# Optimization experiments

Measured on AMD Instinct MI355X. Metric: run time of the kernel, lower is better.

Reference implementation:

```python
import jax, jax.numpy as jnp
import numpy as np

P = 4        # patch_size
H = 16       # num_heads
C = 32       # num_channels
E = C * P ** 3  # embed dim = 2048


def setup_inputs() -> dict:
    key = jax.random.key(0)
    ks = jax.random.split(key, 6)
    s = 0.02
    x = jax.random.normal(ks[0], (4, C, 64, 64, 64), dtype=jnp.float32)
    in_proj_w = jax.random.normal(ks[1], (3 * E, E), dtype=jnp.float32) * s
    in_proj_b = jnp.zeros((3 * E,), dtype=jnp.float32)
    out_proj_w = jax.random.normal(ks[2], (E, E), dtype=jnp.float32) * s
    out_proj_b = jnp.zeros((E,), dtype=jnp.float32)
    mlp_w = jax.random.normal(ks[3], (E, E), dtype=jnp.float32) * s
    mlp_b = jnp.zeros((E,), dtype=jnp.float32)
    return {"x": x, "in_proj_w": in_proj_w, "in_proj_b": in_proj_b,
            "out_proj_w": out_proj_w, "out_proj_b": out_proj_b,
            "mlp_w": mlp_w, "mlp_b": mlp_b}


def reference(x, in_proj_w, in_proj_b, out_proj_w, out_proj_b, mlp_w, mlp_b):
    B, Cc, Rx, Ry, Rz = x.shape
    Nx, Ny, Nz = Rx // P, Ry // P, Rz // P
    N = Nx * Ny * Nz
    hd = E // H

    # --- window partition (torch unfold x3) -> (B, C, Nx, Ny, Nz, px, py, pz)
    xw = x.reshape(B, Cc, Nx, P, Ny, P, Nz, P).transpose(0, 1, 2, 4, 6, 3, 5, 7)
    # -> (B, N, C*p^3); torch then feeds MHA with batch_first=False,
    # so seq_len = B and batch = N (attention mixes across the B axis!)
    tok = xw.reshape(B, Cc, N, P, P, P).transpose(0, 2, 1, 3, 4, 5).reshape(B, N, E)

    # --- multi-head attention (seq = B, batch = N)
    qkv = tok @ in_proj_w.T + in_proj_b            # (B, N, 3E)
    q, k, v = jnp.split(qkv, 3, axis=-1)
    q = q.reshape(B, N, H, hd)
    k = k.reshape(B, N, H, hd)
    v = v.reshape(B, N, H, hd)
    scale = 1.0 / jnp.sqrt(jnp.asarray(hd, dtype=q.dtype))
    scores = jnp.einsum('snhd,tnhd->nhst', q * scale, k)   # (N, H, B, B)
    attn = jax.nn.softmax(scores, axis=-1)
    o = jnp.einsum('nhst,tnhd->snhd', attn, v).reshape(B, N, E)
    o = o @ out_proj_w.T + out_proj_b

    # --- mlp
    o = o @ mlp_w.T + mlp_b

    # --- window reverse, matching the torch.cat-based reassembly:
    # out[b,c, px*Nx+nx, py*Ny+ny, pz*Nz+nz] = x8[b,c,nx,ny,nz,px,py,pz]
    x8 = o.reshape(B, N, Cc, P, P, P).transpose(0, 2, 1, 3, 4, 5)
    x8 = x8.reshape(B, Cc, Nx, Ny, Nz, P, P, P)
    out = x8.transpose(0, 1, 5, 2, 6, 3, 7, 4).reshape(B, Cc, Rx, Ry, Rz)
    return out
```

## Files before the change

### kernel.cpp

```cpp
#include <hip/hip_runtime.h>
#include <stdio.h>


typedef __attribute__((ext_vector_type(4))) float f32x4;
typedef __attribute__((ext_vector_type(8))) short s16x8;
typedef __attribute__((ext_vector_type(2))) unsigned short u16x2;
typedef __attribute__((ext_vector_type(4))) unsigned short u16x4;

#define NB 4
#define NC 32
#define NTOK 4096
#define ED 2048
#define NH 16
#define HD 128

__device__ __forceinline__ unsigned short f2bf(float f) {
    union { float f; unsigned int u; } v; v.f = f;
    unsigned int r = (v.u + 0x7fffu + ((v.u >> 16) & 1u)) >> 16;
    return (unsigned short)r;
}
__device__ __forceinline__ float bf2f(unsigned short u) {
    union { unsigned int u; float f; } v; v.u = ((unsigned int)u) << 16;
    return v.f;
}

#define BARRIER() asm volatile("s_barrier" ::: "memory")
#define LGKM0() do { asm volatile("s_waitcnt lgkmcnt(0)" ::: "memory"); \
                     __builtin_amdgcn_sched_barrier(0); } while (0)
#define VMCNT(n) asm volatile("s_waitcnt vmcnt(" #n ")" ::: "memory")

__global__ void f32_to_bf16_kernel(const float* __restrict__ src,
                                   unsigned short* __restrict__ dst, int n4) {
    int i = blockIdx.x * blockDim.x + threadIdx.x;
    if (i >= n4) return;
    f32x4 v = *(const f32x4*)(src + (size_t)i * 4);
    u16x4 w;
    w.x = f2bf(v.x); w.y = f2bf(v.y); w.z = f2bf(v.z); w.w = f2bf(v.w);
    *(u16x4*)(dst + (size_t)i * 4) = w;
}

__global__ __launch_bounds__(256) void transpose_bf16_kernel(
    const float* __restrict__ src, unsigned short* __restrict__ dst, int n) {
    __shared__ float lds[64][68];
    const int bx = blockIdx.x * 64;
    const int by = blockIdx.y * 64;
    const int t  = threadIdx.x;
    const int r  = t >> 2;
    const int c4 = (t & 3) * 16;
    const float* s = src + (size_t)(by + r) * n + bx + c4;
    #pragma unroll
    for (int i = 0; i < 4; ++i)
        *(f32x4*)&lds[r][c4 + i * 4] = *(const f32x4*)(s + i * 4);
    __syncthreads();
    unsigned short* d = dst + (size_t)(bx + r) * n + by + c4;
    #pragma unroll
    for (int i = 0; i < 4; ++i) {
        u16x4 w;
        w.x = f2bf(lds[c4 + i * 4 + 0][r]);
        w.y = f2bf(lds[c4 + i * 4 + 1][r]);
        w.z = f2bf(lds[c4 + i * 4 + 2][r]);
        w.w = f2bf(lds[c4 + i * 4 + 3][r]);
        *(u16x4*)(d + i * 4) = w;
    }
}

__global__ void bcomb_kernel(const float* __restrict__ mlp_w,
                             const float* __restrict__ opb,
                             const float* __restrict__ mlpb,
                             float* __restrict__ bcomb) {
    int i = blockIdx.x * blockDim.x + threadIdx.x;
    const float* row = mlp_w + (size_t)i * ED;
    float s = 0.0f;
    for (int k = 0; k < ED; k += 4) {
        f32x4 a = *(const f32x4*)(row + k);
        f32x4 b = *(const f32x4*)(opb + k);
        s += a.x * b.x + a.y * b.y + a.z * b.z + a.w * b.w;
    }
    bcomb[i] = s + mlpb[i];
}

__global__ void partition_kernel(const float* __restrict__ x,
                                 unsigned short* __restrict__ tok) {
    int idx = blockIdx.x * blockDim.x + threadIdx.x;
    int m = idx & 15;
    int t = idx >> 4;
    int Y = t & 63; t >>= 6;
    int X = t & 63; t >>= 6;
    int c = t & 31;
    int b = t >> 5;
    f32x4 xv = *(const f32x4*)(x + (size_t)idx * 4);
    int nx = X >> 2, px = X & 3;
    int ny = Y >> 2, py = Y & 3;
    int n = nx * 256 + ny * 16 + m;
    int e = c * 64 + px * 16 + py * 4;
    size_t dst = (size_t)(b * NTOK + n) * ED + e;
    u16x4 w;
    w.x = f2bf(xv.x); w.y = f2bf(xv.y); w.z = f2bf(xv.z); w.w = f2bf(xv.w);
    *(u16x4*)&tok[dst] = w;
}

__global__ __launch_bounds__(256) void gemm128(
    const unsigned short* __restrict__ A,
    const unsigned short* __restrict__ W,
    const float* __restrict__ bias,
    unsigned short* __restrict__ C,
    int M, int Nout, int K)
{
    __shared__ unsigned short ldsA[128 * 64];
    __shared__ unsigned short ldsW[128 * 64];

    const int tid  = threadIdx.x;
    const int wave = tid >> 6;
    const int lane = tid & 63;
    const int bm = blockIdx.x * 128;
    const int bn = blockIdx.y * 128;
    const int wm = (wave >> 1) * 64;
    const int wn = (wave & 1) * 64;

    f32x4 acc[4][4] = {};

    const int srow = lane >> 3;
    const int scol = (lane & 7) * 8;
    const int lrow = lane & 15;
    const int lk   = (lane >> 4) * 8;

    const int nkt = K >> 6;
    for (int kt = 0; kt < nkt; ++kt) {
        const int kbase = kt * 64;
        #pragma unroll
        for (int q = 0; q < 4; ++q) {
            int chunk = wave * 4 + q;
            int row = chunk * 8 + srow;
            const unsigned short* ga = A + (size_t)(bm + row) * K + kbase + scol;
            const unsigned short* gw = W + (size_t)(bn + row) * K + kbase + scol;
            __builtin_amdgcn_global_load_lds(
                (const __attribute__((address_space(1))) void*)ga,
                (__attribute__((address_space(3))) void*)(&ldsA[chunk * 512]),
                16, 0, 0);
            __builtin_amdgcn_global_load_lds(
                (const __attribute__((address_space(1))) void*)gw,
                (__attribute__((address_space(3))) void*)(&ldsW[chunk * 512]),
                16, 0, 0);
        }
        __syncthreads();

        #pragma unroll
        for (int ks = 0; ks < 2; ++ks) {
            const int k0 = ks * 32 + lk;
            s16x8 af[4], bf[4];
            #pragma unroll
            for (int m = 0; m < 4; ++m)
                af[m] = *(const s16x8*)&ldsA[(wm + m * 16 + lrow) * 64 + k0];
            #pragma unroll
            for (int n = 0; n < 4; ++n)
                bf[n] = *(const s16x8*)&ldsW[(wn + n * 16 + lrow) * 64 + k0];
            #pragma unroll
            for (int m = 0; m < 4; ++m)
                #pragma unroll
                for (int n = 0; n < 4; ++n)
                    acc[m][n] = __builtin_amdgcn_mfma_f32_16x16x32_bf16(
                        af[m], bf[n], acc[m][n], 0, 0, 0);
        }
        __syncthreads();
    }

    const int col   = lane & 15;
    const int rbase = (lane >> 4) * 4;
    #pragma unroll
    for (int n = 0; n < 4; ++n) {
        int cc = bn + wn + n * 16 + col;
        float bv = bias[cc];
        #pragma unroll
        for (int m = 0; m < 4; ++m)
            #pragma unroll
            for (int r = 0; r < 4; ++r) {
                int rr = bm + wm + m * 16 + rbase + r;
                C[(size_t)rr * Nout + cc] = f2bf(acc[m][n][r] + bv);
            }
    }
}

template <int OUT_BF16>
__global__ __launch_bounds__(512, 2) void gemm256(
    const unsigned short* __restrict__ A,
    const unsigned short* __restrict__ W,
    const float* __restrict__ bias,
    void* __restrict__ Cv,
    int M, int Nout, int K)
{
    __shared__ unsigned short ldsA[2][2][128 * 64];
    __shared__ unsigned short ldsB[2][2][128 * 64];

    const int tid  = threadIdx.x;
    const int wave = tid >> 6;
    const int lane = tid & 63;

    const int f   = blockIdx.x;
    const int xcd = f & 7;
    const int r_  = f >> 3;
    const int mac = r_ >> 5;
    const int w_  = r_ & 31;
    const int bm  = (xcd * 8 + (w_ & 7)) * 256;
    const int bn  = (mac * 4 + (w_ >> 3)) * 256;

    const int wi    = wave >> 2;
    const int wj    = wave & 3;
    const int bhalf = wj >> 1;
    const int bcol  = (wj & 1) * 64;

    const int lrow = lane & 15;
    const int kq   = lane >> 4;
    const int s0   = ((kq ^ (lrow & 7)) << 3);

    f32x4 acc[8][4] = {};

    const int nkt = K >> 6;

    const int srl   = lane >> 3;
    const int sslot = (((lane & 7) ^ srl) << 3);

    auto stA = [&](int db, int half, int tt) {
        const unsigned short* gb = A + (size_t)(bm + half * 128) * K + tt * 64;
        unsigned short* lb = &ldsA[db][half][0];
        #pragma unroll
        for (int q = 0; q < 2; ++q) {
            const int r0 = wave * 16 + q * 8;
            const unsigned short* ga = gb + (size_t)(r0 + srl) * K + sslot;
            __builtin_amdgcn_global_load_lds(
                (const __attribute__((address_space(1))) void*)ga,
                (__attribute__((address_space(3))) void*)(lb + r0 * 64),
                16, 0, 0);
        }
    };
    auto stB = [&](int db, int half, int tt) {
        const unsigned short* gb = W + (size_t)(bn + half * 128) * K + tt * 64;
        unsigned short* lb = &ldsB[db][half][0];
        #pragma unroll
        for (int q = 0; q < 2; ++q) {
            const int r0 = wave * 16 + q * 8;
            const unsigned short* ga = gb + (size_t)(r0 + srl) * K + sslot;
            __builtin_amdgcn_global_load_lds(
                (const __attribute__((address_space(1))) void*)ga,
                (__attribute__((address_space(3))) void*)(lb + r0 * 64),
                16, 0, 0);
        }
    };

    stA(0, 0, 0); stA(0, 1, 0);
    stB(0, 0, 0); stB(0, 1, 0);
    stA(1, 0, 1); stA(1, 1, 1);
    VMCNT(4);
    BARRIER();

    for (int t = 0; t < nkt; ++t) {
        const int db = t & 1;
        const unsigned short* hA = &ldsA[db][wi][0];
        const unsigned short* hB = &ldsB[db][bhalf][0];

        s16x8 a[8][2], bl[2][2], bh[2][2];

        #pragma unroll
        for (int m = 0; m < 8; ++m) {
            const int rb = (m * 16 + lrow) * 64;
            a[m][0] = *(const s16x8*)&hA[rb + s0];
            a[m][1] = *(const s16x8*)&hA[rb + (s0 ^ 32)];
        }
        #pragma unroll
        for (int n = 0; n < 2; ++n) {
            const int rb = (bcol + n * 16 + lrow) * 64;
            bl[n][0] = *(const s16x8*)&hB[rb + s0];
            bl[n][1] = *(const s16x8*)&hB[rb + (s0 ^ 32)];
        }
        if (t + 1 < nkt) { stB(db ^ 1, 0, t + 1); stB(db ^ 1, 1, t + 1); }
        LGKM0();
        __builtin_amdgcn_s_setprio(1);
        #pragma unroll
        for (int m = 0; m < 8; ++m)
            #pragma unroll
            for (int n = 0; n < 2; ++n) {
                acc[m][n] = __builtin_amdgcn_mfma_f32_16x16x32_bf16(a[m][0], bl[n][0], acc[m][n], 0, 0, 0);
                acc[m][n] = __builtin_amdgcn_mfma_f32_16x16x32_bf16(a[m][1], bl[n][1], acc[m][n], 0, 0, 0);
            }
        __builtin_amdgcn_s_setprio(0);
        BARRIER();

        #pragma unroll
        for (int n = 0; n < 2; ++n) {
            const int rb = (bcol + (n + 2) * 16 + lrow) * 64;
            bh[n][0] = *(const s16x8*)&hB[rb + s0];
            bh[n][1] = *(const s16x8*)&hB[rb + (s0 ^ 32)];
        }
        if (t + 2 < nkt) { stA(db, 0, t + 2); stA(db, 1, t + 2); }
        LGKM0();
        __builtin_amdgcn_s_setprio(1);
        #pragma unroll
        for (int m = 0; m < 8; ++m)
            #pragma unroll
            for (int n = 0; n < 2; ++n) {
                acc[m][n + 2] = __builtin_amdgcn_mfma_f32_16x16x32_bf16(a[m][0], bh[n][0], acc[m][n + 2], 0, 0, 0);
                acc[m][n + 2] = __builtin_amdgcn_mfma_f32_16x16x32_bf16(a[m][1], bh[n][1], acc[m][n + 2], 0, 0, 0);
            }
        __builtin_amdgcn_s_setprio(0);
        if (t + 2 < nkt)      { VMCNT(4); }
        else                  { VMCNT(0); }
        BARRIER();
    }

    const int rowbase = bm + wi * 128 + (kq << 2);
    const int colbase = bn + wj * 64 + lrow;
    float bv[4];
    #pragma unroll
    for (int n = 0; n < 4; ++n) bv[n] = bias[colbase + n * 16];
    #pragma unroll
    for (int m = 0; m < 8; ++m) {
        #pragma unroll
        for (int r = 0; r < 4; ++r) {
            const int rr = rowbase + m * 16 + r;
            #pragma unroll
            for (int n = 0; n < 4; ++n) {
                const int cc = colbase + n * 16;
                const float val = acc[m][n][r] + bv[n];
                if (OUT_BF16)
                    ((unsigned short*)Cv)[(size_t)rr * Nout + cc] = f2bf(val);
                else
                    ((float*)Cv)[(size_t)rr * Nout + cc] = val;
            }
        }
    }
}

__global__ __launch_bounds__(64) void attn_kernel(
    const unsigned short* __restrict__ qkv, unsigned short* __restrict__ o)
{
    const int bid  = blockIdx.x;
    const int n    = bid >> 4;
    const int h    = bid & 15;
    const int lane = threadIdx.x;
    const int d0   = lane * 2;
    const float scale = 0.0883883476483184405501f;

    float q[4][2], k[4][2], v[4][2];
    #pragma unroll
    for (int b = 0; b < 4; ++b) {
        size_t base = (size_t)(b * NTOK + n) * (3 * ED) + h * HD + d0;
        u16x2 uq = *(const u16x2*)&qkv[base];
        u16x2 uk = *(const u16x2*)&qkv[base + ED];
        u16x2 uv = *(const u16x2*)&qkv[base + 2 * ED];
        q[b][0] = bf2f(uq.x); q[b][1] = bf2f(uq.y);
        k[b][0] = bf2f(uk.x); k[b][1] = bf2f(uk.y);
        v[b][0] = bf2f(uv.x); v[b][1] = bf2f(uv.y);
    }

    float sc[4][4];
    #pragma unroll
    for (int s = 0; s < 4; ++s) {
        #pragma unroll
        for (int t = 0; t < 4; ++t) {
            float p = q[s][0] * k[t][0] + q[s][1] * k[t][1];
            #pragma unroll
            for (int off = 32; off > 0; off >>= 1)
                p += __shfl_xor(p, off, 64);
            sc[s][t] = p * scale;
        }
    }

    #pragma unroll
    for (int s = 0; s < 4; ++s) {
        float mx = fmaxf(fmaxf(sc[s][0], sc[s][1]), fmaxf(sc[s][2], sc[s][3]));
        float e0 = __expf(sc[s][0] - mx);
        float e1 = __expf(sc[s][1] - mx);
        float e2 = __expf(sc[s][2] - mx);
        float e3 = __expf(sc[s][3] - mx);
        float inv = 1.0f / (e0 + e1 + e2 + e3);
        float o0 = (e0 * v[0][0] + e1 * v[1][0] + e2 * v[2][0] + e3 * v[3][0]) * inv;
        float o1 = (e0 * v[0][1] + e1 * v[1][1] + e2 * v[2][1] + e3 * v[3][1]) * inv;
        size_t ob = (size_t)(s * NTOK + n) * ED + h * HD + d0;
        u16x2 ov; ov.x = f2bf(o0); ov.y = f2bf(o1);
        *(u16x2*)&o[ob] = ov;
    }
}

__global__ __launch_bounds__(256) void reverse_kernel(const float* __restrict__ o3,
                                                      float* __restrict__ out) {
    __shared__ float lds[16][2052];
    const int t  = threadIdx.x;
    const int b  = blockIdx.x >> 8;
    const int nx = (blockIdx.x >> 4) & 15;
    const int ny = blockIdx.x & 15;
    const int n0 = nx * 256 + ny * 16;

    {
        const int row = t >> 4;
        const int cb  = (t & 15) * 128;
        const float* src = o3 + (size_t)(b * NTOK + n0 + row) * ED + cb;
        #pragma unroll
        for (int i = 0; i < 32; ++i)
            *(f32x4*)&lds[row][cb + i * 4] = *(const f32x4*)&src[i * 4];
    }
    __syncthreads();

    #pragma unroll
    for (int j = 0; j < 2; ++j) {
        const int id = t + j * 256;
        const int py = id & 3, px = (id >> 2) & 3, c = id >> 4;
        const int eb = c * 64 + px * 16 + py * 4;
        f32x4 v[16];
        #pragma unroll
        for (int nz = 0; nz < 16; ++nz)
            v[nz] = *(const f32x4*)&lds[nz][eb];
        float* ob = out + ((size_t)(b * NC + c) * 64 + px * 16 + nx) * 4096
                        + (size_t)(py * 16 + ny) * 64;
        #pragma unroll
        for (int pz = 0; pz < 4; ++pz) {
            float* oz = ob + pz * 16;
            f32x4 w0 = {v[0][pz],  v[1][pz],  v[2][pz],  v[3][pz]};
            f32x4 w1 = {v[4][pz],  v[5][pz],  v[6][pz],  v[7][pz]};
            f32x4 w2 = {v[8][pz],  v[9][pz],  v[10][pz], v[11][pz]};
            f32x4 w3 = {v[12][pz], v[13][pz], v[14][pz], v[15][pz]};
            *(f32x4*)&oz[0]  = w0; *(f32x4*)&oz[4]  = w1;
            *(f32x4*)&oz[8]  = w2; *(f32x4*)&oz[12] = w3;
        }
    }
}

extern "C" void kernel_launch(void* const* d_in, const int* in_sizes, int n_in,
                              void* d_out, int out_size, void* d_ws, size_t ws_size,
                              hipStream_t stream) {
    const float* x          = (const float*)d_in[0];
    const float* in_proj_w  = (const float*)d_in[1];
    const float* in_proj_b  = (const float*)d_in[2];
    const float* out_proj_w = (const float*)d_in[3];
    const float* out_proj_b = (const float*)d_in[4];
    const float* mlp_w      = (const float*)d_in[5];
    const float* mlp_b      = (const float*)d_in[6];
    float* out = (float*)d_out;

    const size_t M = 16384;
    char* ws = (char*)d_ws;
    size_t off = 0;
    unsigned short* tok    = (unsigned short*)(ws + off); off += M * ED * 2;
    unsigned short* w_in   = (unsigned short*)(ws + off); off += (size_t)3 * ED * ED * 2;
    unsigned short* w_mlp  = (unsigned short*)(ws + off); off += (size_t)ED * ED * 2;
    unsigned short* w_outT = (unsigned short*)(ws + off); off += (size_t)ED * ED * 2;
    unsigned short* w_comb = (unsigned short*)(ws + off); off += (size_t)ED * ED * 2;
    float* zbias           = (float*)(ws + off);          off += ED * 4;
    float* b_comb          = (float*)(ws + off);          off += ED * 4;
    unsigned short* obuf   = (unsigned short*)(ws + off); off += M * ED * 2;
    unsigned short* qkv    = (unsigned short*)(ws + off); off += M * 3 * ED * 2;
    float* o3 = (float*)qkv;

    if (ws_size < off) {
        fprintf(stderr, "kernel_launch: ws too small (%zu < %zu)\n", ws_size, off);
        return;
    }

    {
        int n4 = 3 * ED * ED / 4;
        f32_to_bf16_kernel<<<(n4 + 255) / 256, 256, 0, stream>>>(in_proj_w, w_in, n4);
        n4 = ED * ED / 4;
        f32_to_bf16_kernel<<<(n4 + 255) / 256, 256, 0, stream>>>(mlp_w, w_mlp, n4);
        transpose_bf16_kernel<<<dim3(ED / 64, ED / 64), 256, 0, stream>>>(
            out_proj_w, w_outT, ED);
        hipMemsetAsync(zbias, 0, ED * sizeof(float), stream);
    }

    gemm128<<<dim3(ED / 128, ED / 128), 256, 0, stream>>>(
        w_mlp, w_outT, zbias, w_comb, ED, ED, ED);
    bcomb_kernel<<<ED / 256, 256, 0, stream>>>(mlp_w, out_proj_b, mlp_b, b_comb);

    partition_kernel<<<(NB * NC * 64 * 64 * 16) / 256, 256, 0, stream>>>(x, tok);

    gemm256<1><<<dim3(64 * (6144 / 256)), 512, 0, stream>>>(
        tok, w_in, in_proj_b, qkv, 16384, 6144, 2048);

    attn_kernel<<<NTOK * NH, 64, 0, stream>>>(qkv, obuf);

    gemm256<0><<<dim3(64 * (2048 / 256)), 512, 0, stream>>>(
        obuf, w_comb, b_comb, o3, 16384, 2048, 2048);

    reverse_kernel<<<NB * 16 * 16, 256, 0, stream>>>(o3, out);
}
```

Before: 803.0 us.

## Restructure GEMM main loop to prefetch next tile's A fragments during MFMA

Reorganizes the bf16 GEMM inner loop so that A and B tiles for step t+2 are issued together into one double buffer. The low half of the A fragments for the next k-step is loaded from LDS before the second MFMA block, overlapping LDS reads with matrix math. The MFMA work is split by A row halves rather than B column halves, and a partial lgkmcnt wait lets the first MFMAs start while the aHi reads are still in flight. This adds register pressure from the carried aLo fragments, an extra barrier per iteration, and relies on the buffer-reuse ordering staying correct.

```diff
diff --git a/kernel.cpp b/kernel.cpp
--- a/kernel.cpp
+++ b/kernel.cpp
@@ -26,6 +26,8 @@
 
 #define BARRIER() asm volatile("s_barrier" ::: "memory")
 #define LGKM0() do { asm volatile("s_waitcnt lgkmcnt(0)" ::: "memory"); \
+                     __builtin_amdgcn_sched_barrier(0); } while (0)
+#define LGKM8() do { asm volatile("s_waitcnt lgkmcnt(8)" ::: "memory"); \
                      __builtin_amdgcn_sched_barrier(0); } while (0)
 #define VMCNT(n) asm volatile("s_waitcnt vmcnt(" #n ")" ::: "memory")
 
@@ -246,64 +248,98 @@
         }
     };
 
-    stA(0, 0, 0); stA(0, 1, 0);
-    stB(0, 0, 0); stB(0, 1, 0);
-    stA(1, 0, 1); stA(1, 1, 1);
-    VMCNT(4);
+    stA(0, 0, 0); stA(0, 1, 0); stB(0, 0, 0); stB(0, 1, 0);
+    stA(1, 0, 1); stA(1, 1, 1); stB(1, 0, 1); stB(1, 1, 1);
+    VMCNT(8);
     BARRIER();
+
+    s16x8 aLo[4][2];
+    {
+        const unsigned short* hA0 = &ldsA[0][wi][0];
+        #pragma unroll
+        for (int m = 0; m < 4; ++m) {
+            const int rb = (m * 16 + lrow) * 64;
+            aLo[m][0] = *(const s16x8*)&hA0[rb + s0];
+            aLo[m][1] = *(const s16x8*)&hA0[rb + (s0 ^ 32)];
+        }
+    }
 
     for (int t = 0; t < nkt; ++t) {
         const int db = t & 1;
         const unsigned short* hA = &ldsA[db][wi][0];
         const unsigned short* hB = &ldsB[db][bhalf][0];
 
-        s16x8 a[8][2], bl[2][2], bh[2][2];
-
-        #pragma unroll
-        for (int m = 0; m < 8; ++m) {
-            const int rb = (m * 16 + lrow) * 64;
-            a[m][0] = *(const s16x8*)&hA[rb + s0];
-            a[m][1] = *(const s16x8*)&hA[rb + (s0 ^ 32)];
-        }
+        s16x8 aHi[4][2], bl[2][2], bh[2][2];
+
+        LGKM0();
         #pragma unroll
         for (int n = 0; n < 2; ++n) {
             const int rb = (bcol + n * 16 + lrow) * 64;
             bl[n][0] = *(const s16x8*)&hB[rb + s0];
             bl[n][1] = *(const s16x8*)&hB[rb + (s0 ^ 32)];
         }
-        if (t + 1 < nkt) { stB(db ^ 1, 0, t + 1); stB(db ^ 1, 1, t + 1); }
-        LGKM0();
-        __builtin_amdgcn_s_setprio(1);
-        #pragma unroll
-        for (int m = 0; m < 8; ++m)
-            #pragma unroll
-            for (int n = 0; n < 2; ++n) {
-                acc[m][n] = __builtin_amdgcn_mfma_f32_16x16x32_bf16(a[m][0], bl[n][0], acc[m][n], 0, 0, 0);
-                acc[m][n] = __builtin_amdgcn_mfma_f32_16x16x32_bf16(a[m][1], bl[n][1], acc[m][n], 0, 0, 0);
-            }
-        __builtin_amdgcn_s_setprio(0);
-        BARRIER();
-
         #pragma unroll
         for (int n = 0; n < 2; ++n) {
             const int rb = (bcol + (n + 2) * 16 + lrow) * 64;
             bh[n][0] = *(const s16x8*)&hB[rb + s0];
             bh[n][1] = *(const s16x8*)&hB[rb + (s0 ^ 32)];
         }
-        if (t + 2 < nkt) { stA(db, 0, t + 2); stA(db, 1, t + 2); }
-        LGKM0();
+        __builtin_amdgcn_sched_barrier(0);
+        #pragma unroll
+        for (int m = 0; m < 4; ++m) {
+            const int rb = ((m + 4) * 16 + lrow) * 64;
+            aHi[m][0] = *(const s16x8*)&hA[rb + s0];
+            aHi[m][1] = *(const s16x8*)&hA[rb + (s0 ^ 32)];
+        }
+        LGKM8();
+
         __builtin_amdgcn_s_setprio(1);
         #pragma unroll
-        for (int m = 0; m < 8; ++m)
+        for (int m = 0; m < 4; ++m)
             #pragma unroll
             for (int n = 0; n < 2; ++n) {
-                acc[m][n + 2] = __builtin_amdgcn_mfma_f32_16x16x32_bf16(a[m][0], bh[n][0], acc[m][n + 2], 0, 0, 0);
-                acc[m][n + 2] = __builtin_amdgcn_mfma_f32_16x16x32_bf16(a[m][1], bh[n][1], acc[m][n + 2], 0, 0, 0);
+                acc[m][n]     = __builtin_amdgcn_mfma_f32_16x16x32_bf16(aLo[m][0], bl[n][0], acc[m][n], 0, 0, 0);
+                acc[m][n]     = __builtin_amdgcn_mfma_f32_16x16x32_bf16(aLo[m][1], bl[n][1], acc[m][n], 0, 0, 0);
+                acc[m][n + 2] = __builtin_amdgcn_mfma_f32_16x16x32_bf16(aLo[m][0], bh[n][0], acc[m][n + 2], 0, 0, 0);
+                acc[m][n + 2] = __builtin_amdgcn_mfma_f32_16x16x32_bf16(aLo[m][1], bh[n][1], acc[m][n + 2], 0, 0, 0);
             }
         __builtin_amdgcn_s_setprio(0);
-        if (t + 2 < nkt)      { VMCNT(4); }
-        else                  { VMCNT(0); }
+        __builtin_amdgcn_sched_barrier(0);
+
+        LGKM0();
         BARRIER();
+
+        if (t + 2 < nkt) {
+            stA(db, 0, t + 2); stA(db, 1, t + 2);
+            stB(db, 0, t + 2); stB(db, 1, t + 2);
+            VMCNT(8);
+        } else {
+            VMCNT(0);
+        }
+        BARRIER();
+
+        if (t + 1 < nkt) {
+            const unsigned short* hA2 = &ldsA[db ^ 1][wi][0];
+            #pragma unroll
+            for (int m = 0; m < 4; ++m) {
+                const int rb = (m * 16 + lrow) * 64;
+                aLo[m][0] = *(const s16x8*)&hA2[rb + s0];
+                aLo[m][1] = *(const s16x8*)&hA2[rb + (s0 ^ 32)];
+            }
+        }
+        __builtin_amdgcn_sched_barrier(0);
+
+        __builtin_amdgcn_s_setprio(1);
+        #pragma unroll
+        for (int m = 0; m < 4; ++m)
+            #pragma unroll
+            for (int n = 0; n < 2; ++n) {
+                acc[m + 4][n]     = __builtin_amdgcn_mfma_f32_16x16x32_bf16(aHi[m][0], bl[n][0], acc[m + 4][n], 0, 0, 0);
+                acc[m + 4][n]     = __builtin_amdgcn_mfma_f32_16x16x32_bf16(aHi[m][1], bl[n][1], acc[m + 4][n], 0, 0, 0);
+                acc[m + 4][n + 2] = __builtin_amdgcn_mfma_f32_16x16x32_bf16(aHi[m][0], bh[n][0], acc[m + 4][n + 2], 0, 0, 0);
+                acc[m + 4][n + 2] = __builtin_amdgcn_mfma_f32_16x16x32_bf16(aHi[m][1], bh[n][1], acc[m + 4][n + 2], 0, 0, 0);
+            }
+        __builtin_amdgcn_s_setprio(0);
     }
 
     const int rowbase = bm + wi * 128 + (kq << 2);
```

Result: slower. 984.5 us (+22.6%).

## Split gemm256 inner loop into quadrants to overlap LDS reads with MFMA

Applied to the files above, without the earlier changes.

The main K-loop of gemm256 now loads the A fragments in two halves and issues MFMAs in four quadrants. This interleaves LDS reads with matrix math, replacing one lgkmcnt wait and one barrier with scheduling seams, and lowers peak register pressure. Separately, the bias-combination kernel now uses one wave per row with a shuffle reduction instead of one thread per row, giving far more parallelism and coalesced loads. The risk is that the looser waits misorder LDS reads against the asynchronous stores into the other buffer, and that compiler scheduling across the seams turns out worse.

```diff
diff --git a/kernel.cpp b/kernel.cpp
--- a/kernel.cpp
+++ b/kernel.cpp
@@ -28,6 +28,7 @@
 #define LGKM0() do { asm volatile("s_waitcnt lgkmcnt(0)" ::: "memory"); \
                      __builtin_amdgcn_sched_barrier(0); } while (0)
 #define VMCNT(n) asm volatile("s_waitcnt vmcnt(" #n ")" ::: "memory")
+#define SEAM() __builtin_amdgcn_sched_barrier(0)
 
 __global__ void f32_to_bf16_kernel(const float* __restrict__ src,
                                    unsigned short* __restrict__ dst, int n4) {
@@ -64,19 +65,21 @@
     }
 }
 
-__global__ void bcomb_kernel(const float* __restrict__ mlp_w,
-                             const float* __restrict__ opb,
-                             const float* __restrict__ mlpb,
-                             float* __restrict__ bcomb) {
-    int i = blockIdx.x * blockDim.x + threadIdx.x;
-    const float* row = mlp_w + (size_t)i * ED;
+__global__ __launch_bounds__(256) void bcomb_kernel(
+    const float* __restrict__ mlp_w, const float* __restrict__ opb,
+    const float* __restrict__ mlpb, float* __restrict__ bcomb) {
+    const int wave = threadIdx.x >> 6, lane = threadIdx.x & 63;
+    const int row = blockIdx.x * 4 + wave;
+    const float* r = mlp_w + (size_t)row * ED;
     float s = 0.0f;
-    for (int k = 0; k < ED; k += 4) {
-        f32x4 a = *(const f32x4*)(row + k);
+    for (int k = lane * 4; k < ED; k += 256) {
+        f32x4 a = *(const f32x4*)(r + k);
         f32x4 b = *(const f32x4*)(opb + k);
         s += a.x * b.x + a.y * b.y + a.z * b.z + a.w * b.w;
     }
-    bcomb[i] = s + mlpb[i];
+    #pragma unroll
+    for (int off = 32; off > 0; off >>= 1) s += __shfl_xor(s, off, 64);
+    if (lane == 0) bcomb[row] = s + mlpb[row];
 }
 
 __global__ void partition_kernel(const float* __restrict__ x,
@@ -257,13 +260,13 @@
         const unsigned short* hA = &ldsA[db][wi][0];
         const unsigned short* hB = &ldsB[db][bhalf][0];
 
-        s16x8 a[8][2], bl[2][2], bh[2][2];
-
-        #pragma unroll
-        for (int m = 0; m < 8; ++m) {
+        s16x8 aLo[4][2], aHi[4][2], bl[2][2], bh[2][2];
+
+        #pragma unroll
+        for (int m = 0; m < 4; ++m) {
             const int rb = (m * 16 + lrow) * 64;
-            a[m][0] = *(const s16x8*)&hA[rb + s0];
-            a[m][1] = *(const s16x8*)&hA[rb + (s0 ^ 32)];
+            aLo[m][0] = *(const s16x8*)&hA[rb + s0];
+            aLo[m][1] = *(const s16x8*)&hA[rb + (s0 ^ 32)];
         }
         #pragma unroll
         for (int n = 0; n < 2; ++n) {
@@ -272,17 +275,17 @@
             bl[n][1] = *(const s16x8*)&hB[rb + (s0 ^ 32)];
         }
         if (t + 1 < nkt) { stB(db ^ 1, 0, t + 1); stB(db ^ 1, 1, t + 1); }
-        LGKM0();
+        SEAM();
         __builtin_amdgcn_s_setprio(1);
         #pragma unroll
-        for (int m = 0; m < 8; ++m)
+        for (int m = 0; m < 4; ++m)
             #pragma unroll
             for (int n = 0; n < 2; ++n) {
-                acc[m][n] = __builtin_amdgcn_mfma_f32_16x16x32_bf16(a[m][0], bl[n][0], acc[m][n], 0, 0, 0);
-                acc[m][n] = __builtin_amdgcn_mfma_f32_16x16x32_bf16(a[m][1], bl[n][1], acc[m][n], 0, 0, 0);
+                acc[m][n] = __builtin_amdgcn_mfma_f32_16x16x32_bf16(aLo[m][0], bl[n][0], acc[m][n], 0, 0, 0);
+                acc[m][n] = __builtin_amdgcn_mfma_f32_16x16x32_bf16(aLo[m][1], bl[n][1], acc[m][n], 0, 0, 0);
             }
         __builtin_amdgcn_s_setprio(0);
-        BARRIER();
+        SEAM();
 
         #pragma unroll
         for (int n = 0; n < 2; ++n) {
@@ -290,15 +293,44 @@
             bh[n][0] = *(const s16x8*)&hB[rb + s0];
             bh[n][1] = *(const s16x8*)&hB[rb + (s0 ^ 32)];
         }
+        __builtin_amdgcn_s_setprio(1);
+        #pragma unroll
+        for (int m = 0; m < 4; ++m)
+            #pragma unroll
+            for (int n = 0; n < 2; ++n) {
+                acc[m][n + 2] = __builtin_amdgcn_mfma_f32_16x16x32_bf16(aLo[m][0], bh[n][0], acc[m][n + 2], 0, 0, 0);
+                acc[m][n + 2] = __builtin_amdgcn_mfma_f32_16x16x32_bf16(aLo[m][1], bh[n][1], acc[m][n + 2], 0, 0, 0);
+            }
+        __builtin_amdgcn_s_setprio(0);
+        SEAM();
+
+        #pragma unroll
+        for (int m = 0; m < 4; ++m) {
+            const int rb = ((m + 4) * 16 + lrow) * 64;
+            aHi[m][0] = *(const s16x8*)&hA[rb + s0];
+            aHi[m][1] = *(const s16x8*)&hA[rb + (s0 ^ 32)];
+        }
+        LGKM0();
+        BARRIER();
         if (t + 2 < nkt) { stA(db, 0, t + 2); stA(db, 1, t + 2); }
-        LGKM0();
         __builtin_amdgcn_s_setprio(1);
         #pragma unroll
-        for (int m = 0; m < 8; ++m)
+        for (int m = 0; m < 4; ++m)
             #pragma unroll
             for (int n = 0; n < 2; ++n) {
-                acc[m][n + 2] = __builtin_amdgcn_mfma_f32_16x16x32_bf16(a[m][0], bh[n][0], acc[m][n + 2], 0, 0, 0);
-                acc[m][n + 2] = __builtin_amdgcn_mfma_f32_16x16x32_bf16(a[m][1], bh[n][1], acc[m][n + 2], 0, 0, 0);
+                acc[m + 4][n + 2] = __builtin_amdgcn_mfma_f32_16x16x32_bf16(aHi[m][0], bh[n][0], acc[m + 4][n + 2], 0, 0, 0);
+                acc[m + 4][n + 2] = __builtin_amdgcn_mfma_f32_16x16x32_bf16(aHi[m][1], bh[n][1], acc[m + 4][n + 2], 0, 0, 0);
+            }
+        __builtin_amdgcn_s_setprio(0);
+        SEAM();
+
+        __builtin_amdgcn_s_setprio(1);
+        #pragma unroll
+        for (int m = 0; m < 4; ++m)
+            #pragma unroll
+            for (int n = 0; n < 2; ++n) {
+                acc[m + 4][n] = __builtin_amdgcn_mfma_f32_16x16x32_bf16(aHi[m][0], bl[n][0], acc[m + 4][n], 0, 0, 0);
+                acc[m + 4][n] = __builtin_amdgcn_mfma_f32_16x16x32_bf16(aHi[m][1], bl[n][1], acc[m + 4][n], 0, 0, 0);
             }
         __builtin_amdgcn_s_setprio(0);
         if (t + 2 < nkt)      { VMCNT(4); }
@@ -466,7 +498,7 @@
 
     gemm128<<<dim3(ED / 128, ED / 128), 256, 0, stream>>>(
         w_mlp, w_outT, zbias, w_comb, ED, ED, ED);
-    bcomb_kernel<<<ED / 256, 256, 0, stream>>>(mlp_w, out_proj_b, mlp_b, b_comb);
+    bcomb_kernel<<<ED / 4, 256, 0, stream>>>(mlp_w, out_proj_b, mlp_b, b_comb);
 
     partition_kernel<<<(NB * NC * 64 * 64 * 16) / 256, 256, 0, stream>>>(x, tok);
 
```

Result: slower. 823.6 us (+2.6%).

## Fuse window-reverse into final GEMM epilogue and widen attention blocks

Applied to the files above, without the earlier changes.

The final GEMM now writes fp32 results directly into the output volume layout, so the separate reverse kernel and its full intermediate round trip through memory go away. The attention kernel packs 16 heads per 512-thread block with 4-wide bf16 loads and shorter shuffle reductions. The bias-combination kernel uses one wave per row with a shuffle reduction. In exchange, the GEMM epilogue issues scattered 16-byte stores instead of row-contiguous ones.

```diff
diff --git a/kernel.cpp b/kernel.cpp
--- a/kernel.cpp
+++ b/kernel.cpp
@@ -64,19 +64,21 @@
     }
 }
 
-__global__ void bcomb_kernel(const float* __restrict__ mlp_w,
-                             const float* __restrict__ opb,
-                             const float* __restrict__ mlpb,
-                             float* __restrict__ bcomb) {
-    int i = blockIdx.x * blockDim.x + threadIdx.x;
-    const float* row = mlp_w + (size_t)i * ED;
+__global__ __launch_bounds__(256) void bcomb_kernel(
+    const float* __restrict__ mlp_w, const float* __restrict__ opb,
+    const float* __restrict__ mlpb, float* __restrict__ bcomb) {
+    const int wave = threadIdx.x >> 6, lane = threadIdx.x & 63;
+    const int row = blockIdx.x * 4 + wave;
+    const float* r = mlp_w + (size_t)row * ED;
     float s = 0.0f;
-    for (int k = 0; k < ED; k += 4) {
-        f32x4 a = *(const f32x4*)(row + k);
+    for (int k = lane * 4; k < ED; k += 256) {
+        f32x4 a = *(const f32x4*)(r + k);
         f32x4 b = *(const f32x4*)(opb + k);
         s += a.x * b.x + a.y * b.y + a.z * b.z + a.w * b.w;
     }
-    bcomb[i] = s + mlpb[i];
+    #pragma unroll
+    for (int off = 32; off > 0; off >>= 1) s += __shfl_xor(s, off, 64);
+    if (lane == 0) bcomb[row] = s + mlpb[row];
 }
 
 __global__ void partition_kernel(const float* __restrict__ x,
@@ -180,7 +182,7 @@
     }
 }
 
-template <int OUT_BF16>
+template <int OUT_MODE>
 __global__ __launch_bounds__(512, 2) void gemm256(
     const unsigned short* __restrict__ A,
     const unsigned short* __restrict__ W,
@@ -311,44 +313,65 @@
     float bv[4];
     #pragma unroll
     for (int n = 0; n < 4; ++n) bv[n] = bias[colbase + n * 16];
-    #pragma unroll
-    for (int m = 0; m < 8; ++m) {
-        #pragma unroll
-        for (int r = 0; r < 4; ++r) {
-            const int rr = rowbase + m * 16 + r;
-            #pragma unroll
-            for (int n = 0; n < 4; ++n) {
-                const int cc = colbase + n * 16;
-                const float val = acc[m][n][r] + bv[n];
-                if (OUT_BF16)
-                    ((unsigned short*)Cv)[(size_t)rr * Nout + cc] = f2bf(val);
-                else
-                    ((float*)Cv)[(size_t)rr * Nout + cc] = val;
+
+    if (OUT_MODE == 1) {
+        unsigned short* C = (unsigned short*)Cv;
+        #pragma unroll
+        for (int m = 0; m < 8; ++m) {
+            #pragma unroll
+            for (int r = 0; r < 4; ++r) {
+                const int rr = rowbase + m * 16 + r;
+                #pragma unroll
+                for (int n = 0; n < 4; ++n) {
+                    const int cc = colbase + n * 16;
+                    C[(size_t)rr * Nout + cc] = f2bf(acc[m][n][r] + bv[n]);
+                }
             }
         }
-    }
-}
-
-__global__ __launch_bounds__(64) void attn_kernel(
+    } else {
+        float* outp = (float*)Cv;
+        #pragma unroll
+        for (int n = 0; n < 4; ++n) {
+            const int cc = colbase + n * 16;
+            const int c  = cc >> 6, px = (cc >> 4) & 3,
+                      py = (cc >> 2) & 3, pz = cc & 3;
+            #pragma unroll
+            for (int m = 0; m < 8; ++m) {
+                const int rr0 = rowbase + m * 16;
+                const int b   = rr0 >> 12, nx = (rr0 >> 8) & 15,
+                          ny  = (rr0 >> 4) & 15, nz0 = rr0 & 15;
+                float* dst = outp
+                    + ((size_t)((b * NC + c) * 64 + px * 16 + nx)) * 4096
+                    + (size_t)(py * 16 + ny) * 64 + pz * 16 + nz0;
+                f32x4 w = {acc[m][n][0] + bv[n], acc[m][n][1] + bv[n],
+                           acc[m][n][2] + bv[n], acc[m][n][3] + bv[n]};
+                *(f32x4*)dst = w;
+            }
+        }
+    }
+}
+
+__global__ __launch_bounds__(512) void attn_kernel(
     const unsigned short* __restrict__ qkv, unsigned short* __restrict__ o)
 {
-    const int bid  = blockIdx.x;
-    const int n    = bid >> 4;
-    const int h    = bid & 15;
-    const int lane = threadIdx.x;
-    const int d0   = lane * 2;
+    const int n    = blockIdx.x;
+    const int wave = threadIdx.x >> 6;
+    const int lane = threadIdx.x & 63;
+    const int h    = wave * 2 + (lane >> 5);
+    const int dl   = (lane & 31) * 4;
     const float scale = 0.0883883476483184405501f;
 
-    float q[4][2], k[4][2], v[4][2];
+    float q[4][4], k[4][4], v[4][4];
     #pragma unroll
     for (int b = 0; b < 4; ++b) {
-        size_t base = (size_t)(b * NTOK + n) * (3 * ED) + h * HD + d0;
-        u16x2 uq = *(const u16x2*)&qkv[base];
-        u16x2 uk = *(const u16x2*)&qkv[base + ED];
-        u16x2 uv = *(const u16x2*)&qkv[base + 2 * ED];
-        q[b][0] = bf2f(uq.x); q[b][1] = bf2f(uq.y);
-        k[b][0] = bf2f(uk.x); k[b][1] = bf2f(uk.y);
-        v[b][0] = bf2f(uv.x); v[b][1] = bf2f(uv.y);
+        size_t base = (size_t)(b * NTOK + n) * (3 * ED) + h * HD + dl;
+        u16x4 uq = *(const u16x4*)&qkv[base];
+        u16x4 uk = *(const u16x4*)&qkv[base + ED];
+        u16x4 uv = *(const u16x4*)&qkv[base + 2 * ED];
+        #pragma unroll
+        for (int i = 0; i < 4; ++i) {
+            q[b][i] = bf2f(uq[i]); k[b][i] = bf2f(uk[i]); v[b][i] = bf2f(uv[i]);
+        }
     }
 
     float sc[4][4];
@@ -356,9 +379,10 @@
     for (int s = 0; s < 4; ++s) {
         #pragma unroll
         for (int t = 0; t < 4; ++t) {
-            float p = q[s][0] * k[t][0] + q[s][1] * k[t][1];
-            #pragma unroll
-            for (int off = 32; off > 0; off >>= 1)
+            float p = q[s][0] * k[t][0] + q[s][1] * k[t][1]
+                    + q[s][2] * k[t][2] + q[s][3] * k[t][3];
+            #pragma unroll
+            for (int off = 16; off > 0; off >>= 1)
                 p += __shfl_xor(p, off, 64);
             sc[s][t] = p * scale;
         }
@@ -372,54 +396,13 @@
         float e2 = __expf(sc[s][2] - mx);
         float e3 = __expf(sc[s][3] - mx);
         float inv = 1.0f / (e0 + e1 + e2 + e3);
-        float o0 = (e0 * v[0][0] + e1 * v[1][0] + e2 * v[2][0] + e3 * v[3][0]) * inv;
-        float o1 = (e0 * v[0][1] + e1 * v[1][1] + e2 * v[2][1] + e3 * v[3][1]) * inv;
-        size_t ob = (size_t)(s * NTOK + n) * ED + h * HD + d0;
-        u16x2 ov; ov.x = f2bf(o0); ov.y = f2bf(o1);
-        *(u16x2*)&o[ob] = ov;
-    }
-}
-
-__global__ __launch_bounds__(256) void reverse_kernel(const float* __restrict__ o3,
-                                                      float* __restrict__ out) {
-    __shared__ float lds[16][2052];
-    const int t  = threadIdx.x;
-    const int b  = blockIdx.x >> 8;
-    const int nx = (blockIdx.x >> 4) & 15;
-    const int ny = blockIdx.x & 15;
-    const int n0 = nx * 256 + ny * 16;
-
-    {
-        const int row = t >> 4;
-        const int cb  = (t & 15) * 128;
-        const float* src = o3 + (size_t)(b * NTOK + n0 + row) * ED + cb;
-        #pragma unroll
-        for (int i = 0; i < 32; ++i)
-            *(f32x4*)&lds[row][cb + i * 4] = *(const f32x4*)&src[i * 4];
-    }
-    __syncthreads();
-
-    #pragma unroll
-    for (int j = 0; j < 2; ++j) {
-        const int id = t + j * 256;
-        const int py = id & 3, px = (id >> 2) & 3, c = id >> 4;
-        const int eb = c * 64 + px * 16 + py * 4;
-        f32x4 v[16];
-        #pragma unroll
-        for (int nz = 0; nz < 16; ++nz)
-            v[nz] = *(const f32x4*)&lds[nz][eb];
-        float* ob = out + ((size_t)(b * NC + c) * 64 + px * 16 + nx) * 4096
-                        + (size_t)(py * 16 + ny) * 64;
-        #pragma unroll
-        for (int pz = 0; pz < 4; ++pz) {
-            float* oz = ob + pz * 16;
-            f32x4 w0 = {v[0][pz],  v[1][pz],  v[2][pz],  v[3][pz]};
-            f32x4 w1 = {v[4][pz],  v[5][pz],  v[6][pz],  v[7][pz]};
-            f32x4 w2 = {v[8][pz],  v[9][pz],  v[10][pz], v[11][pz]};
-            f32x4 w3 = {v[12][pz], v[13][pz], v[14][pz], v[15][pz]};
-            *(f32x4*)&oz[0]  = w0; *(f32x4*)&oz[4]  = w1;
-            *(f32x4*)&oz[8]  = w2; *(f32x4*)&oz[12] = w3;
-        }
+        u16x4 ov;
+        #pragma unroll
+        for (int i = 0; i < 4; ++i) {
+            float oo = (e0 * v[0][i] + e1 * v[1][i] + e2 * v[2][i] + e3 * v[3][i]) * inv;
+            ov[i] = f2bf(oo);
+        }
+        *(u16x4*)&o[(size_t)(s * NTOK + n) * ED + h * HD + dl] = ov;
     }
 }
 
@@ -447,7 +430,6 @@
     float* b_comb          = (float*)(ws + off);          off += ED * 4;
     unsigned short* obuf   = (unsigned short*)(ws + off); off += M * ED * 2;
     unsigned short* qkv    = (unsigned short*)(ws + off); off += M * 3 * ED * 2;
-    float* o3 = (float*)qkv;
 
     if (ws_size < off) {
         fprintf(stderr, "kernel_launch: ws too small (%zu < %zu)\n", ws_size, off);
@@ -466,17 +448,15 @@
 
     gemm128<<<dim3(ED / 128, ED / 128), 256, 0, stream>>>(
         w_mlp, w_outT, zbias, w_comb, ED, ED, ED);
-    bcomb_kernel<<<ED / 256, 256, 0, stream>>>(mlp_w, out_proj_b, mlp_b, b_comb);
+    bcomb_kernel<<<ED / 4, 256, 0, stream>>>(mlp_w, out_proj_b, mlp_b, b_comb);
 
     partition_kernel<<<(NB * NC * 64 * 64 * 16) / 256, 256, 0, stream>>>(x, tok);
 
     gemm256<1><<<dim3(64 * (6144 / 256)), 512, 0, stream>>>(
         tok, w_in, in_proj_b, qkv, 16384, 6144, 2048);
 
-    attn_kernel<<<NTOK * NH, 64, 0, stream>>>(qkv, obuf);
-
-    gemm256<0><<<dim3(64 * (2048 / 256)), 512, 0, stream>>>(
-        obuf, w_comb, b_comb, o3, 16384, 2048, 2048);
-
-    reverse_kernel<<<NB * 16 * 16, 256, 0, stream>>>(o3, out);
-}
+    attn_kernel<<<NTOK, 512, 0, stream>>>(qkv, obuf);
+
+    gemm256<2><<<dim3(64 * (2048 / 256)), 512, 0, stream>>>(
+        obuf, w_comb, b_comb, out, 16384, 2048, 2048);
+}
```

Result: faster. 666.7 us (-17.0%).
